# Optimization experiments

Hardware: AMD Instinct MI355X
Metric: run time of the kernel (lower is better)

Reference implementation:

```python
import jax, jax.numpy as jnp
import numpy as np

SEQ, BATCH, D_IN, D_LAT = 512, 64, 1024, 1024

def setup_inputs() -> dict:
    key = jax.random.key(0)
    ks = jax.random.split(key, 5)
    scale = 0.02
    d_cat = D_IN + D_LAT
    return {
        "x":   jax.random.normal(ks[0], (SEQ, BATCH, D_IN), dtype=jnp.float32),
        "W_f": jax.random.normal(ks[1], (D_LAT, d_cat), dtype=jnp.float32) * scale,
        "b_f": jnp.zeros((D_LAT,), dtype=jnp.float32),
        "W_i": jax.random.normal(ks[2], (D_LAT, d_cat), dtype=jnp.float32) * scale,
        "b_i": jnp.zeros((D_LAT,), dtype=jnp.float32),
        "W_o": jax.random.normal(ks[3], (D_LAT, d_cat), dtype=jnp.float32) * scale,
        "b_o": jnp.zeros((D_LAT,), dtype=jnp.float32),
        "W_c": jax.random.normal(ks[4], (D_LAT, d_cat), dtype=jnp.float32) * scale,
        "b_c": jnp.zeros((D_LAT,), dtype=jnp.float32),
    }

def reference(x, W_f, b_f, W_i, b_i, W_o, b_o, W_c, b_c):
    # Fuse the 4 gate projections into one GEMM per step (same math).
    d_lat = W_f.shape[0]
    W_all = jnp.concatenate([W_f, W_i, W_o, W_c], axis=0)   # [4*d_lat, d_cat]
    b_all = jnp.concatenate([b_f, b_i, b_o, b_c], axis=0)   # [4*d_lat]
    batch = x.shape[1]
    h0 = jnp.zeros((batch, d_lat), dtype=x.dtype)
    c0 = jnp.zeros((batch, d_lat), dtype=x.dtype)

    def step(carry, x_t):
        h, c = carry
        z = jnp.concatenate([h, x_t], axis=-1)               # [batch, d_lat+d_in]
        gates = z @ W_all.T + b_all                          # [batch, 4*d_lat]
        f_t = jax.nn.sigmoid(gates[:, 0*d_lat:1*d_lat])
        i_t = jax.nn.sigmoid(gates[:, 1*d_lat:2*d_lat])
        o_t = jax.nn.sigmoid(gates[:, 2*d_lat:3*d_lat])
        g_t = jnp.tanh(gates[:, 3*d_lat:4*d_lat])
        c_t = f_t * c + i_t * g_t
        h_t = o_t * jnp.tanh(c_t)
        return (h_t, c_t), h_t

    _, hidden_states = jax.lax.scan(step, (h0, c0), x)       # [seq, batch, d_lat]
    return hidden_states
```

## Files before the change

### kernel.cpp

```cpp
#include <hip/hip_runtime.h>

#define SEQ   512
#define BATCH 64
#define D_IN  1024
#define D_LAT 1024
#define D_CAT 2048
#define NBLK  128
#define JPB   8
#define ROWS  32
#define THREADS 512
#define GPS   67

typedef unsigned short u16;
typedef __attribute__((ext_vector_type(8))) short short8;
typedef __attribute__((ext_vector_type(4))) float floatx4;

__device__ __forceinline__ u16 f2bf(float f) {
    union { float f; unsigned u; } a; a.f = f;
    unsigned u = a.u;
    return (u16)((u + 0x7FFFu + ((u >> 16) & 1u)) >> 16);
}

__device__ __forceinline__ float sigm(float x)  { return 1.0f / (1.0f + __expf(-x)); }
__device__ __forceinline__ float tanhf_(float x){ return 2.0f / (1.0f + __expf(-2.0f * x)) - 1.0f; }

__global__ void cvt_bf16(const float* __restrict__ x, u16* __restrict__ xb, int n8) {
    int i = blockIdx.x * blockDim.x + threadIdx.x;
    int stride = gridDim.x * blockDim.x;
    for (; i < n8; i += stride) {
        float4 v0 = ((const float4*)x)[2 * i];
        float4 v1 = ((const float4*)x)[2 * i + 1];
        short8 o;
        o[0] = (short)f2bf(v0.x); o[1] = (short)f2bf(v0.y);
        o[2] = (short)f2bf(v0.z); o[3] = (short)f2bf(v0.w);
        o[4] = (short)f2bf(v1.x); o[5] = (short)f2bf(v1.y);
        o[6] = (short)f2bf(v1.z); o[7] = (short)f2bf(v1.w);
        *(short8*)(xb + 8 * (size_t)i) = o;
    }
}


__launch_bounds__(THREADS, 2)
__global__ void lstm_persist(const float* __restrict__ Wf, const float* __restrict__ bfp,
                             const float* __restrict__ Wi, const float* __restrict__ bip,
                             const float* __restrict__ Wo, const float* __restrict__ bop,
                             const float* __restrict__ Wc, const float* __restrict__ bcp,
                             const u16* __restrict__ xb,
                             u16* __restrict__ hhist,
                             float* __restrict__ out,
                             unsigned* __restrict__ slots) {
    __shared__ __align__(16) float gp[8][ROWS][GPS];
    __shared__ float biasL[ROWS];
    __shared__ unsigned wdone;

    const int tid  = threadIdx.x;
    const int jblk = blockIdx.x;
    const int c    = tid >> 6;
    const int lane = tid & 63;
    const int m    = lane & 15;
    const int q    = lane >> 4;

    if (tid == 0) wdone = 0u;

    short8 bregH[2][4];
    short8 bregX[2][8];
    #pragma unroll
    for (int rt = 0; rt < 2; ++rt) {
        const int rr  = rt * 16 + m;
        const int g   = rr >> 3;
        const int jj2 = rr & 7;
        const float* Wg = (g == 0) ? Wf : (g == 1) ? Wi : (g == 2) ? Wo : Wc;
        const float* rowp = Wg + (size_t)(jblk * JPB + jj2) * D_CAT;
        #pragma unroll
        for (int ks = 0; ks < 4; ++ks) {
            const float* ph = rowp + c * 128 + ks * 32 + q * 8;
            float4 h0 = *(const float4*)(ph);
            float4 h1 = *(const float4*)(ph + 4);
            short8 bh;
            bh[0] = (short)f2bf(h0.x); bh[1] = (short)f2bf(h0.y);
            bh[2] = (short)f2bf(h0.z); bh[3] = (short)f2bf(h0.w);
            bh[4] = (short)f2bf(h1.x); bh[5] = (short)f2bf(h1.y);
            bh[6] = (short)f2bf(h1.z); bh[7] = (short)f2bf(h1.w);
            bregH[rt][ks] = bh;
        }
        if (c >= 4) {
            #pragma unroll
            for (int ks = 0; ks < 8; ++ks) {
                const float* px = rowp + 1024 + (c - 4) * 256 + ks * 32 + q * 8;
                float4 x0 = *(const float4*)(px);
                float4 x1 = *(const float4*)(px + 4);
                short8 bx;
                bx[0] = (short)f2bf(x0.x); bx[1] = (short)f2bf(x0.y);
                bx[2] = (short)f2bf(x0.z); bx[3] = (short)f2bf(x0.w);
                bx[4] = (short)f2bf(x1.x); bx[5] = (short)f2bf(x1.y);
                bx[6] = (short)f2bf(x1.z); bx[7] = (short)f2bf(x1.w);
                bregX[rt][ks] = bx;
            }
        }
    }
    if (tid < ROWS) {
        const float* bsrc = (tid < 8) ? bfp : (tid < 16) ? bip : (tid < 24) ? bop : bcp;
        biasL[tid] = bsrc[jblk * JPB + (tid & 7)];
    }
    __syncthreads();

    const int cb = tid >> 2;
    const int ca = tid & 3;
    float creg0 = 0.0f, creg1 = 0.0f;

    floatx4 acc[2][4];
    #pragma unroll
    for (int rt = 0; rt < 2; ++rt)
        #pragma unroll
        for (int bt = 0; bt < 4; ++bt)
            acc[rt][bt] = (floatx4){0.f, 0.f, 0.f, 0.f};

    if (c >= 4) {
        const u16* xptr = xb + (size_t)(c - 4) * 256 + q * 8;
        #pragma unroll
        for (int ks = 0; ks < 8; ++ks)
            #pragma unroll
            for (int bt = 0; bt < 4; ++bt) {
                short8 a = *(const short8*)(xptr + (size_t)(bt * 16 + m) * 1024 + ks * 32);
                acc[0][bt] = __builtin_amdgcn_mfma_f32_16x16x32_bf16(a, bregX[0][ks], acc[0][bt], 0, 0, 0);
                acc[1][bt] = __builtin_amdgcn_mfma_f32_16x16x32_bf16(a, bregX[1][ks], acc[1][bt], 0, 0, 0);
            }
    }

    const unsigned* myslot = slots + 16 * c + (lane & 15);

    #pragma unroll 1
    for (int t = 0; t < SEQ; ++t) {
        for (;;) {
            unsigned v = __hip_atomic_load(myslot, __ATOMIC_RELAXED,
                                           __HIP_MEMORY_SCOPE_AGENT);
            if (__all((int)(v >= (unsigned)t))) break;
            __builtin_amdgcn_s_sleep(1);
        }
        asm volatile("" ::: "memory");

        const u16* hptr = hhist + (size_t)t * (BATCH * D_LAT) + c * 128 + q * 8;
        #pragma unroll
        for (int ks = 0; ks < 4; ++ks)
            #pragma unroll
            for (int bt = 0; bt < 4; ++bt) {
                short8 a = *(const short8*)(hptr + (size_t)(bt * 16 + m) * 1024 + ks * 32);
                acc[0][bt] = __builtin_amdgcn_mfma_f32_16x16x32_bf16(a, bregH[0][ks], acc[0][bt], 0, 0, 0);
                acc[1][bt] = __builtin_amdgcn_mfma_f32_16x16x32_bf16(a, bregH[1][ks], acc[1][bt], 0, 0, 0);
            }

        #pragma unroll
        for (int rt = 0; rt < 2; ++rt)
            #pragma unroll
            for (int bt = 0; bt < 4; ++bt)
                #pragma unroll
                for (int r = 0; r < 4; ++r)
                    gp[c][rt * 16 + m][bt * 16 + q * 4 + r] = acc[rt][bt][r];
        __syncthreads();

        if (tid < 256) {
            float h0, h1;
            {
                const int jj = 2 * ca;
                float pf = biasL[jj], pi = biasL[8 + jj], po = biasL[16 + jj], pg = biasL[24 + jj];
                #pragma unroll
                for (int cc = 0; cc < 8; ++cc) {
                    pf += gp[cc][jj][cb];
                    pi += gp[cc][8 + jj][cb];
                    po += gp[cc][16 + jj][cb];
                    pg += gp[cc][24 + jj][cb];
                }
                float ft = sigm(pf), it = sigm(pi), ot = sigm(po), gt = tanhf_(pg);
                creg0 = ft * creg0 + it * gt;
                h0 = ot * tanhf_(creg0);
            }
            {
                const int jj = 2 * ca + 1;
                float pf = biasL[jj], pi = biasL[8 + jj], po = biasL[16 + jj], pg = biasL[24 + jj];
                #pragma unroll
                for (int cc = 0; cc < 8; ++cc) {
                    pf += gp[cc][jj][cb];
                    pi += gp[cc][8 + jj][cb];
                    po += gp[cc][16 + jj][cb];
                    pg += gp[cc][24 + jj][cb];
                }
                float ft = sigm(pf), it = sigm(pi), ot = sigm(po), gt = tanhf_(pg);
                creg1 = ft * creg1 + it * gt;
                h1 = ot * tanhf_(creg1);
            }
            const int jglob = jblk * JPB + 2 * ca;
            unsigned hv = (unsigned)f2bf(h0) | ((unsigned)f2bf(h1) << 16);
            unsigned* hp = (unsigned*)(hhist + (size_t)(t + 1) * (BATCH * D_LAT)
                                             + (size_t)cb * D_LAT + jglob);
            __hip_atomic_store(hp, hv, __ATOMIC_RELAXED, __HIP_MEMORY_SCOPE_AGENT);
            float2 ov = make_float2(h0, h1);
            *(float2*)(out + (size_t)t * (BATCH * D_LAT) + (size_t)cb * D_LAT + jglob) = ov;

            asm volatile("s_waitcnt vmcnt(0)" ::: "memory");
            if (lane == 0) {
                unsigned old = __hip_atomic_fetch_add(&wdone, 1u, __ATOMIC_RELAXED,
                                                      __HIP_MEMORY_SCOPE_WORKGROUP);
                if (old == 4u * (unsigned)t + 3u) {
                    __hip_atomic_store(&slots[jblk], (unsigned)(t + 1),
                                       __ATOMIC_RELAXED, __HIP_MEMORY_SCOPE_AGENT);
                }
            }
            #pragma unroll
            for (int rt = 0; rt < 2; ++rt)
                #pragma unroll
                for (int bt = 0; bt < 4; ++bt)
                    acc[rt][bt] = (floatx4){0.f, 0.f, 0.f, 0.f};
        } else {
            #pragma unroll
            for (int rt = 0; rt < 2; ++rt)
                #pragma unroll
                for (int bt = 0; bt < 4; ++bt)
                    acc[rt][bt] = (floatx4){0.f, 0.f, 0.f, 0.f};
            if (t + 1 < SEQ) {
                const u16* xptr = xb + (size_t)(t + 1) * (BATCH * D_IN) + (c - 4) * 256 + q * 8;
                #pragma unroll
                for (int ks = 0; ks < 8; ++ks)
                    #pragma unroll
                    for (int bt = 0; bt < 4; ++bt) {
                        short8 a = *(const short8*)(xptr + (size_t)(bt * 16 + m) * 1024 + ks * 32);
                        acc[0][bt] = __builtin_amdgcn_mfma_f32_16x16x32_bf16(a, bregX[0][ks], acc[0][bt], 0, 0, 0);
                        acc[1][bt] = __builtin_amdgcn_mfma_f32_16x16x32_bf16(a, bregX[1][ks], acc[1][bt], 0, 0, 0);
                    }
            }
        }

        __syncthreads();
    }
}

extern "C" void kernel_launch(void* const* d_in, const int* in_sizes, int n_in,
                              void* d_out, int out_size, void* d_ws, size_t ws_size,
                              hipStream_t stream) {
    const float* x  = (const float*)d_in[0];
    const float* Wf = (const float*)d_in[1];
    const float* bf = (const float*)d_in[2];
    const float* Wi = (const float*)d_in[3];
    const float* bi = (const float*)d_in[4];
    const float* Wo = (const float*)d_in[5];
    const float* bo = (const float*)d_in[6];
    const float* Wc = (const float*)d_in[7];
    const float* bc = (const float*)d_in[8];
    float* out = (float*)d_out;

    char* ws = (char*)d_ws;
    unsigned* slots = (unsigned*)ws;
    u16* hhist = (u16*)(ws + 1024);
    u16* xb    = (u16*)(ws + 1024 + (size_t)(SEQ + 1) * BATCH * D_LAT * 2);

    hipMemsetAsync(ws, 0, 1024 + (size_t)BATCH * D_LAT * 2, stream);
    cvt_bf16<<<2048, 256, 0, stream>>>(x, xb, SEQ * BATCH * D_IN / 8);
    lstm_persist<<<NBLK, THREADS, 0, stream>>>(Wf, bf, Wi, bi, Wo, bo, Wc, bc,
                                               xb, hhist, out, slots);
}
```

Measured before the change: 4.908 ms.

## Spread pointwise LSTM update over all threads and publish h via single wave

The gate nonlinearity and cell update now use all 512 threads, one (unit, batch) pair each, instead of 256 threads doing two units apiece. The bf16 hidden values are staged in shared memory, and one wavefront packs and stores each batch row's 8 units as 16-byte chunks before setting the block's progress slot. This removes the shared-memory atomic counter and the trailing barrier. It adds an extra __syncthreads for the staging and serialises the global publish through one wave, which could lengthen the critical path of each step.

```diff
diff --git a/kernel.cpp b/kernel.cpp
--- a/kernel.cpp
+++ b/kernel.cpp
@@ -50,8 +50,8 @@
                              float* __restrict__ out,
                              unsigned* __restrict__ slots) {
     __shared__ __align__(16) float gp[8][ROWS][GPS];
+    __shared__ __align__(16) u16 hstage[8][72];
     __shared__ float biasL[ROWS];
-    __shared__ unsigned wdone;
 
     const int tid  = threadIdx.x;
     const int jblk = blockIdx.x;
@@ -59,8 +59,6 @@
     const int lane = tid & 63;
     const int m    = lane & 15;
     const int q    = lane >> 4;
-
-    if (tid == 0) wdone = 0u;
 
     short8 bregH[2][4];
     short8 bregX[2][8];
@@ -104,9 +102,7 @@
     }
     __syncthreads();
 
-    const int cb = tid >> 2;
-    const int ca = tid & 3;
-    float creg0 = 0.0f, creg1 = 0.0f;
+    float creg = 0.0f;
 
     floatx4 acc[2][4];
     #pragma unroll
@@ -156,80 +152,60 @@
                 #pragma unroll
                 for (int r = 0; r < 4; ++r)
                     gp[c][rt * 16 + m][bt * 16 + q * 4 + r] = acc[rt][bt][r];
+        #pragma unroll
+        for (int rt = 0; rt < 2; ++rt)
+            #pragma unroll
+            for (int bt = 0; bt < 4; ++bt)
+                acc[rt][bt] = (floatx4){0.f, 0.f, 0.f, 0.f};
         __syncthreads();
 
-        if (tid < 256) {
-            float h0, h1;
-            {
-                const int jj = 2 * ca;
-                float pf = biasL[jj], pi = biasL[8 + jj], po = biasL[16 + jj], pg = biasL[24 + jj];
-                #pragma unroll
-                for (int cc = 0; cc < 8; ++cc) {
-                    pf += gp[cc][jj][cb];
-                    pi += gp[cc][8 + jj][cb];
-                    po += gp[cc][16 + jj][cb];
-                    pg += gp[cc][24 + jj][cb];
-                }
-                float ft = sigm(pf), it = sigm(pi), ot = sigm(po), gt = tanhf_(pg);
-                creg0 = ft * creg0 + it * gt;
-                h0 = ot * tanhf_(creg0);
-            }
-            {
-                const int jj = 2 * ca + 1;
-                float pf = biasL[jj], pi = biasL[8 + jj], po = biasL[16 + jj], pg = biasL[24 + jj];
-                #pragma unroll
-                for (int cc = 0; cc < 8; ++cc) {
-                    pf += gp[cc][jj][cb];
-                    pi += gp[cc][8 + jj][cb];
-                    po += gp[cc][16 + jj][cb];
-                    pg += gp[cc][24 + jj][cb];
-                }
-                float ft = sigm(pf), it = sigm(pi), ot = sigm(po), gt = tanhf_(pg);
-                creg1 = ft * creg1 + it * gt;
-                h1 = ot * tanhf_(creg1);
-            }
-            const int jglob = jblk * JPB + 2 * ca;
-            unsigned hv = (unsigned)f2bf(h0) | ((unsigned)f2bf(h1) << 16);
-            unsigned* hp = (unsigned*)(hhist + (size_t)(t + 1) * (BATCH * D_LAT)
-                                             + (size_t)cb * D_LAT + jglob);
-            __hip_atomic_store(hp, hv, __ATOMIC_RELAXED, __HIP_MEMORY_SCOPE_AGENT);
-            float2 ov = make_float2(h0, h1);
-            *(float2*)(out + (size_t)t * (BATCH * D_LAT) + (size_t)cb * D_LAT + jglob) = ov;
-
+        float hf;
+        {
+            const int jj = c;
+            const int b  = lane;
+            float pf = biasL[jj], pi = biasL[8 + jj], po = biasL[16 + jj], pg = biasL[24 + jj];
+            #pragma unroll
+            for (int cc = 0; cc < 8; ++cc) {
+                pf += gp[cc][jj][b];
+                pi += gp[cc][8 + jj][b];
+                po += gp[cc][16 + jj][b];
+                pg += gp[cc][24 + jj][b];
+            }
+            float ft = sigm(pf), it = sigm(pi), ot = sigm(po), gt = tanhf_(pg);
+            creg = ft * creg + it * gt;
+            hf = ot * tanhf_(creg);
+            hstage[jj][b] = f2bf(hf);
+        }
+        __syncthreads();
+
+        if (c == 0) {
+            union { short8 s; unsigned long long u[2]; } pk;
+            #pragma unroll
+            for (int j = 0; j < 8; ++j) pk.s[j] = (short)hstage[j][lane];
+            unsigned long long* hp = (unsigned long long*)
+                (hhist + (size_t)(t + 1) * (BATCH * D_LAT) + (size_t)lane * D_LAT + jblk * JPB);
+            __hip_atomic_store(&hp[0], pk.u[0], __ATOMIC_RELAXED, __HIP_MEMORY_SCOPE_AGENT);
+            __hip_atomic_store(&hp[1], pk.u[1], __ATOMIC_RELAXED, __HIP_MEMORY_SCOPE_AGENT);
             asm volatile("s_waitcnt vmcnt(0)" ::: "memory");
             if (lane == 0) {
-                unsigned old = __hip_atomic_fetch_add(&wdone, 1u, __ATOMIC_RELAXED,
-                                                      __HIP_MEMORY_SCOPE_WORKGROUP);
-                if (old == 4u * (unsigned)t + 3u) {
-                    __hip_atomic_store(&slots[jblk], (unsigned)(t + 1),
-                                       __ATOMIC_RELAXED, __HIP_MEMORY_SCOPE_AGENT);
+                __hip_atomic_store(&slots[jblk], (unsigned)(t + 1),
+                                   __ATOMIC_RELAXED, __HIP_MEMORY_SCOPE_AGENT);
+            }
+        }
+
+        out[(size_t)t * (BATCH * D_LAT) + (size_t)lane * D_LAT + jblk * JPB + c] = hf;
+
+        if (c >= 4 && t + 1 < SEQ) {
+            const u16* xptr = xb + (size_t)(t + 1) * (BATCH * D_IN) + (c - 4) * 256 + q * 8;
+            #pragma unroll
+            for (int ks = 0; ks < 8; ++ks)
+                #pragma unroll
+                for (int bt = 0; bt < 4; ++bt) {
+                    short8 a = *(const short8*)(xptr + (size_t)(bt * 16 + m) * 1024 + ks * 32);
+                    acc[0][bt] = __builtin_amdgcn_mfma_f32_16x16x32_bf16(a, bregX[0][ks], acc[0][bt], 0, 0, 0);
+                    acc[1][bt] = __builtin_amdgcn_mfma_f32_16x16x32_bf16(a, bregX[1][ks], acc[1][bt], 0, 0, 0);
                 }
-            }
-            #pragma unroll
-            for (int rt = 0; rt < 2; ++rt)
-                #pragma unroll
-                for (int bt = 0; bt < 4; ++bt)
-                    acc[rt][bt] = (floatx4){0.f, 0.f, 0.f, 0.f};
-        } else {
-            #pragma unroll
-            for (int rt = 0; rt < 2; ++rt)
-                #pragma unroll
-                for (int bt = 0; bt < 4; ++bt)
-                    acc[rt][bt] = (floatx4){0.f, 0.f, 0.f, 0.f};
-            if (t + 1 < SEQ) {
-                const u16* xptr = xb + (size_t)(t + 1) * (BATCH * D_IN) + (c - 4) * 256 + q * 8;
-                #pragma unroll
-                for (int ks = 0; ks < 8; ++ks)
-                    #pragma unroll
-                    for (int bt = 0; bt < 4; ++bt) {
-                        short8 a = *(const short8*)(xptr + (size_t)(bt * 16 + m) * 1024 + ks * 32);
-                        acc[0][bt] = __builtin_amdgcn_mfma_f32_16x16x32_bf16(a, bregX[0][ks], acc[0][bt], 0, 0, 0);
-                        acc[1][bt] = __builtin_amdgcn_mfma_f32_16x16x32_bf16(a, bregX[1][ks], acc[1][bt], 0, 0, 0);
-                    }
-            }
-        }
-
-        __syncthreads();
+        }
     }
 }
 
```

New measurement: 5.688 ms. 15.9% more time.

## Replace per-block flag barrier with poison-value dataflow sync on h history

Applied to the files above, without the earlier changes.

Removes the slot counters and the workgroup atomic counting. Each h value slot is pre-filled with a NaN-pattern poison word, and consumers spin on the h fragments themselves until no poison remains. Each block re-poisons the slot for step t+2 before writing step t+1, so the history buffer can be reused without global flags. This cuts the flag round-trip latency from the recurrent critical path and lets consumers start as soon as their specific fragments arrive. The cost is per-fragment polling loads, and correctness relies on ordering and on real outputs never matching the poison bit pattern.

```diff
diff --git a/kernel.cpp b/kernel.cpp
--- a/kernel.cpp
+++ b/kernel.cpp
@@ -10,8 +10,10 @@
 #define ROWS  32
 #define THREADS 512
 #define GPS   67
+#define POIS  0x7FC07FC0u
 
 typedef unsigned short u16;
+typedef unsigned long long u64;
 typedef __attribute__((ext_vector_type(8))) short short8;
 typedef __attribute__((ext_vector_type(4))) float floatx4;
 
@@ -24,9 +26,12 @@
 __device__ __forceinline__ float sigm(float x)  { return 1.0f / (1.0f + __expf(-x)); }
 __device__ __forceinline__ float tanhf_(float x){ return 2.0f / (1.0f + __expf(-2.0f * x)) - 1.0f; }
 
-__global__ void cvt_bf16(const float* __restrict__ x, u16* __restrict__ xb, int n8) {
+__global__ void cvt_bf16(const float* __restrict__ x, u16* __restrict__ xb,
+                         u16* __restrict__ hhist, int n8) {
     int i = blockIdx.x * blockDim.x + threadIdx.x;
     int stride = gridDim.x * blockDim.x;
+    unsigned* p1 = (unsigned*)(hhist + (size_t)BATCH * D_LAT);
+    for (int j = i; j < BATCH * D_LAT / 2; j += stride) p1[j] = POIS;
     for (; i < n8; i += stride) {
         float4 v0 = ((const float4*)x)[2 * i];
         float4 v1 = ((const float4*)x)[2 * i + 1];
@@ -47,11 +52,9 @@
                              const float* __restrict__ Wc, const float* __restrict__ bcp,
                              const u16* __restrict__ xb,
                              u16* __restrict__ hhist,
-                             float* __restrict__ out,
-                             unsigned* __restrict__ slots) {
+                             float* __restrict__ out) {
     __shared__ __align__(16) float gp[8][ROWS][GPS];
     __shared__ float biasL[ROWS];
-    __shared__ unsigned wdone;
 
     const int tid  = threadIdx.x;
     const int jblk = blockIdx.x;
@@ -59,8 +62,6 @@
     const int lane = tid & 63;
     const int m    = lane & 15;
     const int q    = lane >> 4;
-
-    if (tid == 0) wdone = 0u;
 
     short8 bregH[2][4];
     short8 bregX[2][8];
@@ -127,26 +128,35 @@
             }
     }
 
-    const unsigned* myslot = slots + 16 * c + (lane & 15);
-
     #pragma unroll 1
     for (int t = 0; t < SEQ; ++t) {
-        for (;;) {
-            unsigned v = __hip_atomic_load(myslot, __ATOMIC_RELAXED,
-                                           __HIP_MEMORY_SCOPE_AGENT);
-            if (__all((int)(v >= (unsigned)t))) break;
-            __builtin_amdgcn_s_sleep(1);
-        }
-        asm volatile("" ::: "memory");
-
-        const u16* hptr = hhist + (size_t)t * (BATCH * D_LAT) + c * 128 + q * 8;
+        const u16* hbase = hhist + (size_t)t * (BATCH * D_LAT) + c * 128 + q * 8;
+        union Fr { u64 u[2]; short8 s; };
+        Fr fr[4][4];
         #pragma unroll
         for (int ks = 0; ks < 4; ++ks)
             #pragma unroll
             for (int bt = 0; bt < 4; ++bt) {
-                short8 a = *(const short8*)(hptr + (size_t)(bt * 16 + m) * 1024 + ks * 32);
-                acc[0][bt] = __builtin_amdgcn_mfma_f32_16x16x32_bf16(a, bregH[0][ks], acc[0][bt], 0, 0, 0);
-                acc[1][bt] = __builtin_amdgcn_mfma_f32_16x16x32_bf16(a, bregH[1][ks], acc[1][bt], 0, 0, 0);
+                const u64* p = (const u64*)(hbase + (size_t)(bt * 16 + m) * 1024 + ks * 32);
+                fr[ks][bt].u[0] = __hip_atomic_load(&p[0], __ATOMIC_RELAXED, __HIP_MEMORY_SCOPE_AGENT);
+                fr[ks][bt].u[1] = __hip_atomic_load(&p[1], __ATOMIC_RELAXED, __HIP_MEMORY_SCOPE_AGENT);
+            }
+        #pragma unroll
+        for (int ks = 0; ks < 4; ++ks)
+            #pragma unroll
+            for (int bt = 0; bt < 4; ++bt) {
+                const u64* p = (const u64*)(hbase + (size_t)(bt * 16 + m) * 1024 + ks * 32);
+                for (;;) {
+                    u64 a0 = fr[ks][bt].u[0], a1 = fr[ks][bt].u[1];
+                    int bad = ((unsigned)a0 == POIS) | ((unsigned)(a0 >> 32) == POIS)
+                            | ((unsigned)a1 == POIS) | ((unsigned)(a1 >> 32) == POIS);
+                    if (!__any(bad)) break;
+                    __builtin_amdgcn_s_sleep(1);
+                    fr[ks][bt].u[0] = __hip_atomic_load(&p[0], __ATOMIC_RELAXED, __HIP_MEMORY_SCOPE_AGENT);
+                    fr[ks][bt].u[1] = __hip_atomic_load(&p[1], __ATOMIC_RELAXED, __HIP_MEMORY_SCOPE_AGENT);
+                }
+                acc[0][bt] = __builtin_amdgcn_mfma_f32_16x16x32_bf16(fr[ks][bt].s, bregH[0][ks], acc[0][bt], 0, 0, 0);
+                acc[1][bt] = __builtin_amdgcn_mfma_f32_16x16x32_bf16(fr[ks][bt].s, bregH[1][ks], acc[1][bt], 0, 0, 0);
             }
 
         #pragma unroll
@@ -159,6 +169,12 @@
         __syncthreads();
 
         if (tid < 256) {
+            const int jglob = jblk * JPB + 2 * ca;
+            if (t + 2 <= SEQ) {
+                unsigned* pp = (unsigned*)(hhist + (size_t)(t + 2) * (BATCH * D_LAT)
+                                                 + (size_t)cb * D_LAT + jglob);
+                __hip_atomic_store(pp, POIS, __ATOMIC_RELAXED, __HIP_MEMORY_SCOPE_AGENT);
+            }
             float h0, h1;
             {
                 const int jj = 2 * ca;
@@ -188,23 +204,13 @@
                 creg1 = ft * creg1 + it * gt;
                 h1 = ot * tanhf_(creg1);
             }
-            const int jglob = jblk * JPB + 2 * ca;
+            asm volatile("s_waitcnt vmcnt(0)" ::: "memory");
             unsigned hv = (unsigned)f2bf(h0) | ((unsigned)f2bf(h1) << 16);
             unsigned* hp = (unsigned*)(hhist + (size_t)(t + 1) * (BATCH * D_LAT)
                                              + (size_t)cb * D_LAT + jglob);
             __hip_atomic_store(hp, hv, __ATOMIC_RELAXED, __HIP_MEMORY_SCOPE_AGENT);
             float2 ov = make_float2(h0, h1);
             *(float2*)(out + (size_t)t * (BATCH * D_LAT) + (size_t)cb * D_LAT + jglob) = ov;
-
-            asm volatile("s_waitcnt vmcnt(0)" ::: "memory");
-            if (lane == 0) {
-                unsigned old = __hip_atomic_fetch_add(&wdone, 1u, __ATOMIC_RELAXED,
-                                                      __HIP_MEMORY_SCOPE_WORKGROUP);
-                if (old == 4u * (unsigned)t + 3u) {
-                    __hip_atomic_store(&slots[jblk], (unsigned)(t + 1),
-                                       __ATOMIC_RELAXED, __HIP_MEMORY_SCOPE_AGENT);
-                }
-            }
             #pragma unroll
             for (int rt = 0; rt < 2; ++rt)
                 #pragma unroll
@@ -248,12 +254,11 @@
     float* out = (float*)d_out;
 
     char* ws = (char*)d_ws;
-    unsigned* slots = (unsigned*)ws;
     u16* hhist = (u16*)(ws + 1024);
     u16* xb    = (u16*)(ws + 1024 + (size_t)(SEQ + 1) * BATCH * D_LAT * 2);
 
     hipMemsetAsync(ws, 0, 1024 + (size_t)BATCH * D_LAT * 2, stream);
-    cvt_bf16<<<2048, 256, 0, stream>>>(x, xb, SEQ * BATCH * D_IN / 8);
+    cvt_bf16<<<2048, 256, 0, stream>>>(x, xb, hhist, SEQ * BATCH * D_IN / 8);
     lstm_persist<<<NBLK, THREADS, 0, stream>>>(Wf, bf, Wi, bi, Wo, bo, Wc, bc,
-                                               xb, hhist, out, slots);
-}
+                                               xb, hhist, out);
+}
```

Measured after the change: 7.252 ms. 47.8% more time.
